# Kernel optimization log

Measured on AMD Instinct MI355X. Metric: run time of the kernel, lower is better.

The kernel has to match this reference:

```python
import jax, jax.numpy as jnp
import numpy as np

N_QUBITS = 12
DIM = 2 ** N_QUBITS  # 4096

_H = (jnp.array([[1.0, 1.0], [1.0, -1.0]]) / np.sqrt(2.0)).astype(jnp.complex64)
_X = jnp.array([[0.0, 1.0], [1.0, 0.0]], dtype=jnp.complex64)


def setup_inputs() -> dict:
    key = jax.random.key(0)
    k1, k2 = jax.random.split(key)
    state = jax.random.normal(k1, (8, 512, DIM), dtype=jnp.float32)
    params = jax.random.normal(k2, (N_QUBITS,), dtype=jnp.float32)
    return {"state": state, "params": params}


def _to_quantum(x):
    # faithful to _classical_to_quantum_inspired: normalize, phase = acos(|v|), sign * exp(i*phase)
    norms = jnp.linalg.norm(x, axis=-1, keepdims=True)
    v = x / (norms + 1e-8)
    mag = jnp.minimum(jnp.abs(v), 1.0)
    q = (jnp.sign(v) * jnp.exp(1j * jnp.arccos(mag))).astype(jnp.complex64)
    nrm = jnp.sqrt(jnp.sum(q.real ** 2 + q.imag ** 2, axis=-1, keepdims=True))
    return q / nrm.astype(jnp.complex64)


def _axis(q):
    # qubit q = bit q (LSB); tensor axes ordered MSB-first after batch axis 0
    return 1 + (N_QUBITS - 1 - q)


def _apply_1q(full, q, U):
    ax = _axis(q)
    moved = jnp.moveaxis(full, ax, -1)
    out = jnp.einsum('...b,ab->...a', moved, U)
    return jnp.moveaxis(out, -1, ax)


def _apply_ctrl(full, c, t, U):
    # apply U on target qubit t where control qubit c == 1
    axc = _axis(c)
    b0 = jnp.take(full, 0, axis=axc)
    b1 = jnp.take(full, 1, axis=axc)
    axt = _axis(t)
    axt_sub = axt - 1 if axt > axc else axt
    moved = jnp.moveaxis(b1, axt_sub, -1)
    b1n = jnp.moveaxis(jnp.einsum('...b,ab->...a', moved, U), -1, axt_sub)
    return jnp.stack([b0, b1n], axis=axc)


def _rx(theta):
    c = jnp.cos(theta / 2).astype(jnp.complex64)
    s = (-1j * jnp.sin(theta / 2)).astype(jnp.complex64)
    return jnp.stack([jnp.stack([c, s]), jnp.stack([s, c])])


def reference(state, params):
    B, T, D = state.shape
    psi = _to_quantum(state.reshape(B * T, D))  # (N, 2**n) complex64
    full = psi.reshape((B * T,) + (2,) * N_QUBITS)
    for q in range(N_QUBITS):
        full = _apply_1q(full, q, _H)                                  # Hadamard
        full = _apply_ctrl(full, q, (q + 1) % N_QUBITS, _rx(params[q]))  # controlled-RX
        if q < N_QUBITS - 1:
            full = _apply_ctrl(full, q, q + 1, _X)                     # CNOT
    amp = full.reshape(B * T, D)
    probs = amp.real ** 2 + amp.imag ** 2  # measurement probabilities
    return probs.reshape(B, T, D).astype(jnp.float32)
```

## Files before the change

kernel.cpp:

```cpp
#include <hip/hip_runtime.h>

#define NQ  12
#define DIM 4096
#define TPB 256

typedef float v2f __attribute__((ext_vector_type(2)));
typedef float v4f __attribute__((ext_vector_type(4)));


__device__ __forceinline__ float wave_reduce(float v) {
#pragma unroll
    for (int m = 32; m >= 1; m >>= 1) v += __shfl_xor(v, m, 64);
    return v;
}

#define BCAST(v, q) __uint_as_float(__builtin_amdgcn_readlane(__float_as_uint(v), (q)))

template <int MC, int MT, bool XGATE>
__device__ __forceinline__ void apply_layer(v2f* a, v2f ctv, v2f snv) {
#pragma unroll
    for (int i = 0; i < 16; ++i) {
        if (i & MC) continue;
        const int j = i | MC;
        const v2f t0 = a[i], t1 = a[j];
        a[i] = t0 + t1;
        a[j] = t0 - t1;
    }
#pragma unroll
    for (int i = 0; i < 16; ++i) {
        if (!(i & MC) || (i & MT)) continue;
        const int j = i | MT;
        const v2f b0 = a[i], b1 = a[j];
        const v2f s0 = snv * b0.yx;
        const v2f s1 = snv * b1.yx;
        if (XGATE) {
            a[i] = ctv * b1 + s0;
            a[j] = ctv * b0 + s1;
        } else {
            a[i] = ctv * b0 + s1;
            a[j] = ctv * b1 + s0;
        }
    }
}

__global__ __launch_bounds__(TPB, 5) void qlayer_kernel(
        const float* __restrict__ state, const float* __restrict__ params,
        float* __restrict__ out) {
    __shared__ __align__(16) v2f amp[DIM];
    char* const lds = (char*)amp;

    const int t = threadIdx.x;
    const int lane = t & 63;
    const long long sbase = (long long)blockIdx.x * DIM;

    const float th = params[lane < NQ ? lane : 0] * 0.5f;
    const float cl = cosf(th);
    const float sl = sinf(th);

    const float4* gp = (const float4*)(state + sbase);
    float4 xv[4];
    float ss = 0.f;
#pragma unroll
    for (int j = 0; j < 4; ++j) {
        const float4 v = gp[t + 256 * j];
        xv[j] = v;
        ss = fmaf(v.x, v.x, ss); ss = fmaf(v.y, v.y, ss);
        ss = fmaf(v.z, v.z, ss); ss = fmaf(v.w, v.w, ss);
    }
    const int stbase = 16 * (t ^ ((t >> 3) & 7));
#pragma unroll
    for (int j = 0; j < 4; ++j)
        *(v4f*)(lds + stbase + (j << 12)) = (v4f){xv[j].x, xv[j].y, xv[j].z, xv[j].w};

    ss = wave_reduce(ss);
    if (lane == 0) ((float*)lds)[4096 + (t >> 6)] = ss;
    __syncthreads();
    const float* redp = (const float*)lds + 4096;
    const float nrm  = sqrtf(redp[0] + redp[1] + redp[2] + redp[3]);
    const float invd = 1.0f / (nrm + 1e-8f);

    const int A = (64 * t ^ (((t >> 3) & 1) << 6)) | (((t >> 1) & 3) << 4);
    float4 x4[4];
#pragma unroll
    for (int j = 0; j < 4; ++j)
        x4[j] = *(const float4*)(lds + (A ^ (j << 4)));
    __syncthreads();

    v2f a[16];
#define ENC(k, xval)                                                      \
    {                                                                     \
        const float v   = (xval) * invd;                                  \
        const float re  = fminf(fmaxf(v, -1.0f), 1.0f);                   \
        const float imb = __builtin_amdgcn_sqrtf(fmaxf(1.0f - re * re, 0.f)); \
        const float im  = (v > 0.f) ? imb : ((v < 0.f) ? -imb : 0.f);     \
        v2f q; q.x = re; q.y = im;                                        \
        a[k] = q;                                                         \
    }
#pragma unroll
    for (int j = 0; j < 4; ++j) {
        const float4 xq = x4[j];
        ENC(4 * j + 0, xq.x); ENC(4 * j + 1, xq.y);
        ENC(4 * j + 2, xq.z); ENC(4 * j + 3, xq.w);
    }
#undef ENC

#define CTV(q) ({ v2f _c; _c.x = BCAST(cl, q); _c.y = _c.x; _c; })
#define SNV(q) ({ float _s = BCAST(sl, q); v2f _v; _v.x = _s; _v.y = -_s; _v; })

    apply_layer<1, 2, true>(a, CTV(0), SNV(0));
    apply_layer<2, 4, true>(a, CTV(1), SNV(1));
    apply_layer<4, 8, true>(a, CTV(2), SNV(2));
    {
        const int v1b = (t << 7) | (((t >> 1) & 7) << 4);
#pragma unroll
        for (int k = 0; k < 8; ++k) {
            v4f w; w.x = a[2 * k].x; w.y = a[2 * k].y;
            w.z = a[2 * k + 1].x; w.w = a[2 * k + 1].y;
            *(v4f*)(lds + (v1b ^ (k << 4))) = w;
        }
    }
    __syncthreads();

    {
        const int g  = t >> 3;
        const int gp2 = g & 1;
        const int baseE = ((t & 7) << 3) + (g << 10) + (gp2 << 6);
        const int baseO = ((t & 7) << 3) + (g << 10) + ((1 - gp2) << 6);
#pragma unroll
        for (int r = 0; r < 16; ++r)
            a[r] = *(const v2f*)(lds +
                ((((r & 1) ? baseO : baseE) ^ ((r >> 2) << 4)) + ((r >> 1) << 7)));
        apply_layer<1, 2, true>(a, CTV(3), SNV(3));
        apply_layer<2, 4, true>(a, CTV(4), SNV(4));
        apply_layer<4, 8, true>(a, CTV(5), SNV(5));
#pragma unroll
        for (int r = 0; r < 16; ++r)
            *(v2f*)(lds +
                ((((r & 1) ? baseO : baseE) ^ ((r >> 2) << 4)) + ((r >> 1) << 7))) = a[r];
    }
    __syncthreads();

    {
        const int b3b = (((t & 63) ^ (((t >> 5) & 1) << 1)) << 3) + ((t >> 6) << 13);
#pragma unroll
        for (int r = 0; r < 16; ++r)
            a[r] = *(const v2f*)(lds + ((b3b ^ ((r & 3) << 5)) + (r << 9)));
        apply_layer<1, 2, true>(a, CTV(6), SNV(6));
        apply_layer<2, 4, true>(a, CTV(7), SNV(7));
        apply_layer<4, 8, true>(a, CTV(8), SNV(8));
#pragma unroll
        for (int r = 0; r < 16; ++r)
            *(v2f*)(lds + ((b3b ^ ((r & 3) << 5)) + (r << 9))) = a[r];
    }
    __syncthreads();

    {
        const int F0b = (t << 4) ^ (((t >> 4) & 7) << 4);
#pragma unroll
        for (int k = 0; k < 8; ++k) {
            const v4f v = *(const v4f*)(lds + (F0b + (k << 12)));
            v2f q0; q0.x = v.x; q0.y = v.y;
            v2f q1; q1.x = v.z; q1.y = v.w;
            a[k] = q0;
            a[k + 8] = q1;
        }
        apply_layer<1, 2, true >(a, CTV(9),  SNV(9));
        apply_layer<2, 4, true >(a, CTV(10), SNV(10));
        apply_layer<4, 8, false>(a, CTV(11), SNV(11));

        v2f sc2; sc2.x = 0x1p-24f; sc2.y = 0x1p-24f;
        v2f* outp = (v2f*)(out + sbase);
#pragma unroll
        for (int k = 0; k < 8; ++k) {
            const v2f q0 = a[k] * a[k];
            const v2f q1 = a[k | 8] * a[k | 8];
            v2f res; res.x = q0.x + q0.y;
            res.y = q1.x + q1.y;
            res = res * sc2;
            __builtin_nontemporal_store(res, outp + t + (k << 8));
        }
    }
#undef CTV
#undef SNV
}

extern "C" void kernel_launch(void* const* d_in, const int* in_sizes, int n_in,
                              void* d_out, int out_size, void* d_ws, size_t ws_size,
                              hipStream_t stream) {
    (void)in_sizes; (void)n_in; (void)out_size; (void)d_ws; (void)ws_size;
    const float* state  = (const float*)d_in[0];
    const float* params = (const float*)d_in[1];
    float* out = (float*)d_out;
    qlayer_kernel<<<dim3(4096), dim3(TPB), 0, stream>>>(state, params, out);
}
```

Before: 118.3 us.

## Process 32 amplitudes per thread with 128 threads and three gate passes

Halves the block to 128 threads so each thread holds 32 complex amplitudes and applies four qubit layers per register pass. This cuts the LDS exchange rounds from four to three and drops the initial LDS transpose, since each thread loads 32 contiguous inputs directly. The cost is higher register pressure, lower occupancy (launch bound of 2 blocks), and per-thread strided global loads that coalesce less well.

```diff
diff --git a/kernel.cpp b/kernel.cpp
--- a/kernel.cpp
+++ b/kernel.cpp
@@ -2,7 +2,7 @@
 
 #define NQ  12
 #define DIM 4096
-#define TPB 256
+#define TPB 128
 
 typedef float v2f __attribute__((ext_vector_type(2)));
 typedef float v4f __attribute__((ext_vector_type(4)));
@@ -19,7 +19,7 @@
 template <int MC, int MT, bool XGATE>
 __device__ __forceinline__ void apply_layer(v2f* a, v2f ctv, v2f snv) {
 #pragma unroll
-    for (int i = 0; i < 16; ++i) {
+    for (int i = 0; i < 32; ++i) {
         if (i & MC) continue;
         const int j = i | MC;
         const v2f t0 = a[i], t1 = a[j];
@@ -27,7 +27,7 @@
         a[j] = t0 - t1;
     }
 #pragma unroll
-    for (int i = 0; i < 16; ++i) {
+    for (int i = 0; i < 32; ++i) {
         if (!(i & MC) || (i & MT)) continue;
         const int j = i | MT;
         const v2f b0 = a[i], b1 = a[j];
@@ -43,7 +43,7 @@
     }
 }
 
-__global__ __launch_bounds__(TPB, 5) void qlayer_kernel(
+__global__ __launch_bounds__(TPB, 2) void qlayer_kernel(
         const float* __restrict__ state, const float* __restrict__ params,
         float* __restrict__ out) {
     __shared__ __align__(16) v2f amp[DIM];
@@ -57,36 +57,24 @@
     const float cl = cosf(th);
     const float sl = sinf(th);
 
-    const float4* gp = (const float4*)(state + sbase);
-    float4 xv[4];
+    const float4* gp = (const float4*)(state + sbase + t * 32);
+    float4 xv[8];
     float ss = 0.f;
 #pragma unroll
-    for (int j = 0; j < 4; ++j) {
-        const float4 v = gp[t + 256 * j];
+    for (int j = 0; j < 8; ++j) {
+        const float4 v = gp[j];
         xv[j] = v;
         ss = fmaf(v.x, v.x, ss); ss = fmaf(v.y, v.y, ss);
         ss = fmaf(v.z, v.z, ss); ss = fmaf(v.w, v.w, ss);
     }
-    const int stbase = 16 * (t ^ ((t >> 3) & 7));
-#pragma unroll
-    for (int j = 0; j < 4; ++j)
-        *(v4f*)(lds + stbase + (j << 12)) = (v4f){xv[j].x, xv[j].y, xv[j].z, xv[j].w};
-
     ss = wave_reduce(ss);
-    if (lane == 0) ((float*)lds)[4096 + (t >> 6)] = ss;
+    if (lane == 0) ((float*)lds)[t >> 6] = ss;
     __syncthreads();
-    const float* redp = (const float*)lds + 4096;
-    const float nrm  = sqrtf(redp[0] + redp[1] + redp[2] + redp[3]);
+    const float nrm  = sqrtf(((const float*)lds)[0] + ((const float*)lds)[1]);
     const float invd = 1.0f / (nrm + 1e-8f);
-
-    const int A = (64 * t ^ (((t >> 3) & 1) << 6)) | (((t >> 1) & 3) << 4);
-    float4 x4[4];
-#pragma unroll
-    for (int j = 0; j < 4; ++j)
-        x4[j] = *(const float4*)(lds + (A ^ (j << 4)));
     __syncthreads();
 
-    v2f a[16];
+    v2f a[32];
 #define ENC(k, xval)                                                      \
     {                                                                     \
         const float v   = (xval) * invd;                                  \
@@ -97,8 +85,8 @@
         a[k] = q;                                                         \
     }
 #pragma unroll
-    for (int j = 0; j < 4; ++j) {
-        const float4 xq = x4[j];
+    for (int j = 0; j < 8; ++j) {
+        const float4 xq = xv[j];
         ENC(4 * j + 0, xq.x); ENC(4 * j + 1, xq.y);
         ENC(4 * j + 2, xq.z); ENC(4 * j + 3, xq.w);
     }
@@ -107,77 +95,62 @@
 #define CTV(q) ({ v2f _c; _c.x = BCAST(cl, q); _c.y = _c.x; _c; })
 #define SNV(q) ({ float _s = BCAST(sl, q); v2f _v; _v.x = _s; _v.y = -_s; _v; })
 
-    apply_layer<1, 2, true>(a, CTV(0), SNV(0));
-    apply_layer<2, 4, true>(a, CTV(1), SNV(1));
-    apply_layer<4, 8, true>(a, CTV(2), SNV(2));
+    apply_layer<1,  2, true>(a, CTV(0), SNV(0));
+    apply_layer<2,  4, true>(a, CTV(1), SNV(1));
+    apply_layer<4,  8, true>(a, CTV(2), SNV(2));
+    apply_layer<8, 16, true>(a, CTV(3), SNV(3));
+
     {
-        const int v1b = (t << 7) | (((t >> 1) & 7) << 4);
+        const int base1 = (t << 8) | ((t & 7) << 4);
 #pragma unroll
-        for (int k = 0; k < 8; ++k) {
-            v4f w; w.x = a[2 * k].x; w.y = a[2 * k].y;
+        for (int k = 0; k < 16; ++k) {
+            v4f w; w.x = a[2 * k].x;     w.y = a[2 * k].y;
             w.z = a[2 * k + 1].x; w.w = a[2 * k + 1].y;
-            *(v4f*)(lds + (v1b ^ (k << 4))) = w;
+            *(v4f*)(lds + (base1 ^ (k << 4))) = w;
         }
     }
     __syncthreads();
 
-    {
-        const int g  = t >> 3;
-        const int gp2 = g & 1;
-        const int baseE = ((t & 7) << 3) + (g << 10) + (gp2 << 6);
-        const int baseO = ((t & 7) << 3) + (g << 10) + ((1 - gp2) << 6);
+    const int B2 = ((t & 15) << 3) + ((t >> 4) << 12);
 #pragma unroll
-        for (int r = 0; r < 16; ++r)
-            a[r] = *(const v2f*)(lds +
-                ((((r & 1) ? baseO : baseE) ^ ((r >> 2) << 4)) + ((r >> 1) << 7)));
-        apply_layer<1, 2, true>(a, CTV(3), SNV(3));
-        apply_layer<2, 4, true>(a, CTV(4), SNV(4));
-        apply_layer<4, 8, true>(a, CTV(5), SNV(5));
+    for (int r = 0; r < 32; ++r)
+        a[r] = *(const v2f*)(lds + ((B2 ^ (((r >> 1) & 7) << 4)) + (r << 7)));
+
+    apply_layer<1,  2, true>(a, CTV(4), SNV(4));
+    apply_layer<2,  4, true>(a, CTV(5), SNV(5));
+    apply_layer<4,  8, true>(a, CTV(6), SNV(6));
+    apply_layer<8, 16, true>(a, CTV(7), SNV(7));
+
 #pragma unroll
-        for (int r = 0; r < 16; ++r)
-            *(v2f*)(lds +
-                ((((r & 1) ? baseO : baseE) ^ ((r >> 2) << 4)) + ((r >> 1) << 7))) = a[r];
-    }
+    for (int r = 0; r < 32; ++r)
+        *(v2f*)(lds + ((B2 ^ (((r >> 1) & 7) << 4)) + (r << 7))) = a[r];
     __syncthreads();
 
     {
-        const int b3b = (((t & 63) ^ (((t >> 5) & 1) << 1)) << 3) + ((t >> 6) << 13);
+        const int F = (t << 4) ^ (((t >> 4) & 7) << 4);
 #pragma unroll
-        for (int r = 0; r < 16; ++r)
-            a[r] = *(const v2f*)(lds + ((b3b ^ ((r & 3) << 5)) + (r << 9)));
-        apply_layer<1, 2, true>(a, CTV(6), SNV(6));
-        apply_layer<2, 4, true>(a, CTV(7), SNV(7));
-        apply_layer<4, 8, true>(a, CTV(8), SNV(8));
-#pragma unroll
-        for (int r = 0; r < 16; ++r)
-            *(v2f*)(lds + ((b3b ^ ((r & 3) << 5)) + (r << 9))) = a[r];
-    }
-    __syncthreads();
-
-    {
-        const int F0b = (t << 4) ^ (((t >> 4) & 7) << 4);
-#pragma unroll
-        for (int k = 0; k < 8; ++k) {
-            const v4f v = *(const v4f*)(lds + (F0b + (k << 12)));
+        for (int rh = 0; rh < 16; ++rh) {
+            const v4f v = *(const v4f*)(lds + (F + (rh << 11)));
             v2f q0; q0.x = v.x; q0.y = v.y;
             v2f q1; q1.x = v.z; q1.y = v.w;
-            a[k] = q0;
-            a[k + 8] = q1;
+            a[rh]      = q0;
+            a[rh + 16] = q1;
         }
-        apply_layer<1, 2, true >(a, CTV(9),  SNV(9));
-        apply_layer<2, 4, true >(a, CTV(10), SNV(10));
-        apply_layer<4, 8, false>(a, CTV(11), SNV(11));
+        apply_layer<1,  2, true >(a, CTV(8),  SNV(8));
+        apply_layer<2,  4, true >(a, CTV(9),  SNV(9));
+        apply_layer<4,  8, true >(a, CTV(10), SNV(10));
+        apply_layer<8, 16, false>(a, CTV(11), SNV(11));
 
         v2f sc2; sc2.x = 0x1p-24f; sc2.y = 0x1p-24f;
         v2f* outp = (v2f*)(out + sbase);
 #pragma unroll
-        for (int k = 0; k < 8; ++k) {
-            const v2f q0 = a[k] * a[k];
-            const v2f q1 = a[k | 8] * a[k | 8];
+        for (int rh = 0; rh < 16; ++rh) {
+            const v2f q0 = a[rh] * a[rh];
+            const v2f q1 = a[rh + 16] * a[rh + 16];
             v2f res; res.x = q0.x + q0.y;
             res.y = q1.x + q1.y;
             res = res * sc2;
-            __builtin_nontemporal_store(res, outp + t + (k << 8));
+            __builtin_nontemporal_store(res, outp + t + (rh << 7));
         }
     }
 #undef CTV
```

New measurement: 121.6 us. 1.03x slower.

## Load contiguous 16 amplitudes per thread and use 128-bit swizzled LDS exchanges

Applied to the files above, without the earlier changes.

Each thread now loads 16 contiguous floats straight from global memory, which removes the initial LDS staging round-trip and one barrier's worth of shuffle traffic. All inter-stage LDS exchanges are reworked to use 16-byte vector reads and writes with XOR swizzles in place of 8-byte scalar accesses. The aim is fewer LDS instructions and bank conflicts. The trade-off is that the global loads are now strided per thread rather than fully coalesced across the wave.

```diff
diff --git a/kernel.cpp b/kernel.cpp
--- a/kernel.cpp
+++ b/kernel.cpp
@@ -57,33 +57,22 @@
     const float cl = cosf(th);
     const float sl = sinf(th);
 
-    const float4* gp = (const float4*)(state + sbase);
+    const float4* gp = (const float4*)(state + sbase + t * 16);
     float4 xv[4];
     float ss = 0.f;
 #pragma unroll
     for (int j = 0; j < 4; ++j) {
-        const float4 v = gp[t + 256 * j];
+        const float4 v = gp[j];
         xv[j] = v;
         ss = fmaf(v.x, v.x, ss); ss = fmaf(v.y, v.y, ss);
         ss = fmaf(v.z, v.z, ss); ss = fmaf(v.w, v.w, ss);
     }
-    const int stbase = 16 * (t ^ ((t >> 3) & 7));
-#pragma unroll
-    for (int j = 0; j < 4; ++j)
-        *(v4f*)(lds + stbase + (j << 12)) = (v4f){xv[j].x, xv[j].y, xv[j].z, xv[j].w};
-
     ss = wave_reduce(ss);
-    if (lane == 0) ((float*)lds)[4096 + (t >> 6)] = ss;
-    __syncthreads();
-    const float* redp = (const float*)lds + 4096;
+    if (lane == 0) ((float*)lds)[t >> 6] = ss;
+    __syncthreads();
+    const float* redp = (const float*)lds;
     const float nrm  = sqrtf(redp[0] + redp[1] + redp[2] + redp[3]);
     const float invd = 1.0f / (nrm + 1e-8f);
-
-    const int A = (64 * t ^ (((t >> 3) & 1) << 6)) | (((t >> 1) & 3) << 4);
-    float4 x4[4];
-#pragma unroll
-    for (int j = 0; j < 4; ++j)
-        x4[j] = *(const float4*)(lds + (A ^ (j << 4)));
     __syncthreads();
 
     v2f a[16];
@@ -98,7 +87,7 @@
     }
 #pragma unroll
     for (int j = 0; j < 4; ++j) {
-        const float4 xq = x4[j];
+        const float4 xq = xv[j];
         ENC(4 * j + 0, xq.x); ENC(4 * j + 1, xq.y);
         ENC(4 * j + 2, xq.z); ENC(4 * j + 3, xq.w);
     }
@@ -106,63 +95,80 @@
 
 #define CTV(q) ({ v2f _c; _c.x = BCAST(cl, q); _c.y = _c.x; _c; })
 #define SNV(q) ({ float _s = BCAST(sl, q); v2f _v; _v.x = _s; _v.y = -_s; _v; })
+
+    const int c1 = (t & 7) ^ ((t >> 3) & 7);
 
     apply_layer<1, 2, true>(a, CTV(0), SNV(0));
     apply_layer<2, 4, true>(a, CTV(1), SNV(1));
     apply_layer<4, 8, true>(a, CTV(2), SNV(2));
     {
-        const int v1b = (t << 7) | (((t >> 1) & 7) << 4);
-#pragma unroll
-        for (int k = 0; k < 8; ++k) {
-            v4f w; w.x = a[2 * k].x; w.y = a[2 * k].y;
-            w.z = a[2 * k + 1].x; w.w = a[2 * k + 1].y;
-            *(v4f*)(lds + (v1b ^ (k << 4))) = w;
-        }
-    }
-    __syncthreads();
-
-    {
-        const int g  = t >> 3;
-        const int gp2 = g & 1;
-        const int baseE = ((t & 7) << 3) + (g << 10) + (gp2 << 6);
-        const int baseO = ((t & 7) << 3) + (g << 10) + ((1 - gp2) << 6);
-#pragma unroll
-        for (int r = 0; r < 16; ++r)
-            a[r] = *(const v2f*)(lds +
-                ((((r & 1) ? baseO : baseE) ^ ((r >> 2) << 4)) + ((r >> 1) << 7)));
+        const int base1 = (t << 7) | (c1 << 4);
+#pragma unroll
+        for (int p = 0; p < 8; ++p) {
+            v4f w; w.x = a[p].x;     w.y = a[p].y;
+            w.z = a[p + 8].x; w.w = a[p + 8].y;
+            *(v4f*)(lds + (base1 ^ (p << 4))) = w;
+        }
+    }
+    __syncthreads();
+
+    {
+        const int g = t >> 3;
+        const int base2 = (c1 << 4) | (g << 10);
+#pragma unroll
+        for (int m = 0; m < 8; ++m) {
+            const v4f v = *(const v4f*)(lds + (base2 ^ ((m << 7) | (m << 4))));
+            v2f q0; q0.x = v.x; q0.y = v.y;
+            v2f q1; q1.x = v.z; q1.y = v.w;
+            a[2 * m]     = q0;
+            a[2 * m + 1] = q1;
+        }
         apply_layer<1, 2, true>(a, CTV(3), SNV(3));
         apply_layer<2, 4, true>(a, CTV(4), SNV(4));
         apply_layer<4, 8, true>(a, CTV(5), SNV(5));
 #pragma unroll
-        for (int r = 0; r < 16; ++r)
-            *(v2f*)(lds +
-                ((((r & 1) ? baseO : baseE) ^ ((r >> 2) << 4)) + ((r >> 1) << 7))) = a[r];
-    }
-    __syncthreads();
-
-    {
-        const int b3b = (((t & 63) ^ (((t >> 5) & 1) << 1)) << 3) + ((t >> 6) << 13);
-#pragma unroll
-        for (int r = 0; r < 16; ++r)
-            a[r] = *(const v2f*)(lds + ((b3b ^ ((r & 3) << 5)) + (r << 9)));
+        for (int p = 0; p < 8; ++p) {
+            v4f w; w.x = a[p].x;     w.y = a[p].y;
+            w.z = a[p + 8].x; w.w = a[p + 8].y;
+            *(v4f*)(lds + (base2 ^ ((p << 7) | (p << 4)))) = w;
+        }
+    }
+    __syncthreads();
+
+    {
+        const int base3 = (((t & 63) ^ ((t >> 3) & 7)) << 4) + ((t >> 6) << 13);
+#pragma unroll
+        for (int m = 0; m < 8; ++m) {
+            const v4f v = *(const v4f*)(lds + (base3 ^ ((m << 10) | (m << 4))));
+            v2f q0; q0.x = v.x; q0.y = v.y;
+            v2f q1; q1.x = v.z; q1.y = v.w;
+            a[2 * m]     = q0;
+            a[2 * m + 1] = q1;
+        }
         apply_layer<1, 2, true>(a, CTV(6), SNV(6));
         apply_layer<2, 4, true>(a, CTV(7), SNV(7));
         apply_layer<4, 8, true>(a, CTV(8), SNV(8));
 #pragma unroll
-        for (int r = 0; r < 16; ++r)
-            *(v2f*)(lds + ((b3b ^ ((r & 3) << 5)) + (r << 9))) = a[r];
-    }
-    __syncthreads();
-
-    {
-        const int F0b = (t << 4) ^ (((t >> 4) & 7) << 4);
-#pragma unroll
-        for (int k = 0; k < 8; ++k) {
-            const v4f v = *(const v4f*)(lds + (F0b + (k << 12)));
-            v2f q0; q0.x = v.x; q0.y = v.y;
-            v2f q1; q1.x = v.z; q1.y = v.w;
-            a[k] = q0;
-            a[k + 8] = q1;
+        for (int p = 0; p < 8; ++p) {
+            v4f w; w.x = a[p].x;     w.y = a[p].y;
+            w.z = a[p + 8].x; w.w = a[p + 8].y;
+            *(v4f*)(lds + (base3 ^ ((p << 10) | (p << 4)))) = w;
+        }
+    }
+    __syncthreads();
+
+    {
+        const int c4 = ((t >> 2) & 7) ^ ((t >> 5) & 7);
+        const int base40 = (t << 5) ^ (c4 << 4);
+        const int base41 = base40 ^ 16;
+#pragma unroll
+        for (int j = 0; j < 4; ++j) {
+            const v4f v0 = *(const v4f*)(lds + base40 + (j << 13));
+            const v4f v1 = *(const v4f*)(lds + base41 + (j << 13));
+            v2f q; q.x = v0.x; q.y = v0.y; a[2 * j]         = q;
+            q.x = v0.z; q.y = v0.w;        a[2 * j + 1]     = q;
+            q.x = v1.x; q.y = v1.y;        a[2 * j + 8]     = q;
+            q.x = v1.z; q.y = v1.w;        a[2 * j + 9]     = q;
         }
         apply_layer<1, 2, true >(a, CTV(9),  SNV(9));
         apply_layer<2, 4, true >(a, CTV(10), SNV(10));
```

After: 115.6 us. -2.3%, faster.
